# Kernel tuning notes

Measured on AMD Instinct MI355X. Metric: run time of the kernel, lower is better.

Reference implementation:

```python
import jax, jax.numpy as jnp
import numpy as np

N_CB = 10          # n_codebooks
K = 2048           # codebook_size
D = 256            # codebook_dim
SEM = 256          # semantic_proj_dim
W2V = 1024         # w2v_bert_dim
COMMIT = 0.25      # commitment_cost


def setup_inputs() -> dict:
    key = jax.random.key(0)
    ks = jax.random.split(key, 7)
    B, T = 16, 1024
    z = jax.random.normal(ks[0], (B, T, D), jnp.float32)
    w2v_targets = jax.random.normal(ks[1], (B, T, W2V), jnp.float32)
    # codebooks: uniform(-1/K, 1/K) as in nn.init.uniform_
    E = jax.random.uniform(ks[2], (N_CB, K, D), jnp.float32, -1.0 / K, 1.0 / K)
    # semantic head: Linear(D, SEM) -> GELU -> Linear(SEM, W2V)
    W1 = jax.random.normal(ks[3], (D, SEM), jnp.float32) * (1.0 / np.sqrt(D))
    b1 = jnp.zeros((SEM,), jnp.float32)
    W2 = jax.random.normal(ks[4], (SEM, W2V), jnp.float32) * (1.0 / np.sqrt(SEM))
    b2 = jnp.zeros((W2V,), jnp.float32)
    return {"z": z, "w2v_targets": w2v_targets, "E": E,
            "W1": W1, "b1": b1, "W2": W2, "b2": b2}


def _vq_step(residual, Ei):
    """Single-codebook VQ with straight-through estimator.
    residual: (B,T,D); Ei: (K,D). Returns (z_q, indices, loss)."""
    sg = jax.lax.stop_gradient
    B, T, d = residual.shape
    flat = residual.reshape(-1, d)                      # (N, D)
    dist = (jnp.sum(flat * flat, axis=1, keepdims=True)
            - 2.0 * flat @ Ei.T
            + jnp.sum(Ei * Ei, axis=1))
    idx = jnp.argmin(dist, axis=1).reshape(B, T)        # (B, T)
    q = Ei[idx]                                         # (B, T, D) gather
    commitment_loss = jnp.mean((sg(q) - residual) ** 2)
    embedding_loss = jnp.mean((q - sg(residual)) ** 2)
    loss = embedding_loss + COMMIT * commitment_loss
    z_q = residual + sg(q - residual)                   # straight-through
    return z_q, idx, loss


def reference(z, w2v_targets, E, W1, b1, W2, b2):
    residual = z
    z_q_total = jnp.zeros_like(z)
    codes = []
    vq_loss = jnp.float32(0.0)
    semantic_loss = jnp.float32(0.0)
    for i in range(N_CB):
        z_q_i, idx_i, loss_i = _vq_step(residual, E[i])
        if i == 0:
            # semantic head on CB1 output (torch GELU default = exact erf)
            h = jax.nn.gelu(z_q_i @ W1 + b1, approximate=False)
            predicted = h @ W2 + b2                     # (B, T, W2V)
            semantic_loss = jnp.mean((predicted - w2v_targets) ** 2)
        z_q_total = z_q_total + z_q_i
        residual = residual - jax.lax.stop_gradient(z_q_i)
        vq_loss = vq_loss + loss_i
        codes.append(idx_i)
    all_codes = jnp.stack(codes, axis=-1)               # (B, T, N_CB)
    return z_q_total, all_codes, vq_loss, semantic_loss
```

## Files before the change

### kernel.cpp

```cpp
#include <hip/hip_runtime.h>
#include <float.h>
#include <math.h>

#define NTOK 16384
#define KCB  2048
#define DDIM 256
#define NCB  10
#define MARGIN 5.0e-4f

typedef __attribute__((ext_vector_type(8))) short  short8;
typedef __attribute__((ext_vector_type(4))) float  f32x4;

static __device__ __forceinline__ unsigned short f2bf(float f) {
    unsigned int b = __float_as_uint(f);
    unsigned int r = b + 0x7FFFu + ((b >> 16) & 1u);
    return (unsigned short)(r >> 16);
}

__global__ __launch_bounds__(256) void prep_all(const float* __restrict__ E,
                                                const float* __restrict__ z,
                                                const float* __restrict__ W1,
                                                const float* __restrict__ W2,
                                                float* __restrict__ sseE,
                                                float* __restrict__ normA,
                                                unsigned short* __restrict__ Eh,
                                                unsigned short* __restrict__ resH,
                                                unsigned short* __restrict__ w1t,
                                                unsigned short* __restrict__ w2t) {
    const int b = blockIdx.x;
    if (b < 9216) {
        const float* src; unsigned short* dst; int i;
        if (b < 5120) { src = E; dst = Eh;   i = b * 256 + threadIdx.x; }
        else          { src = z; dst = resH; i = (b - 5120) * 256 + threadIdx.x; }
        float4 f = *(const float4*)(src + (size_t)i * 4);
        unsigned short h[4] = { f2bf(f.x), f2bf(f.y), f2bf(f.z), f2bf(f.w) };
        *(ushort4*)(dst + (size_t)i * 4) = *(ushort4*)h;
    } else if (b < 9472) {
        int j = (b - 9216) * 256 + threadIdx.x;
        int n = j >> 8, k = j & 255;
        w1t[j] = f2bf(W1[k * 256 + n]);
    } else if (b < 10496) {
        int j = (b - 9472) * 256 + threadIdx.x;
        int n = j >> 8, k = j & 255;
        w2t[j] = f2bf(W2[k * 1024 + n]);
    } else {
        const int gw   = ((b - 10496) * 256 + threadIdx.x) >> 6;
        const int lane = threadIdx.x & 63;
        const int row  = gw * 4 + (lane >> 4);
        const int l    = lane & 15;
        const float* src = nullptr; float* dst = nullptr;
        if (row < NCB * KCB)             { src = E + (size_t)row * DDIM;               dst = sseE + row; }
        else if (row < NCB * KCB + NTOK) { src = z + (size_t)(row - NCB * KCB) * DDIM; dst = normA + (row - NCB * KCB); }
        float r = 0.f;
        if (src) {
            const float* a = src + ((l >> 3) << 7) + (l & 7);
            float v = a[0];
            r = __fmul_rn(v, v);
            #pragma unroll
            for (int k = 1; k < 16; ++k) { v = a[k * 8]; r = __fadd_rn(r, __fmul_rn(v, v)); }
        }
        r = __fadd_rn(r, __shfl_xor(r, 1, 64));
        r = __fadd_rn(r, __shfl_xor(r, 2, 64));
        r = __fadd_rn(r, __shfl_xor(r, 4, 64));
        r = __fadd_rn(r, __shfl_xor(r, 8, 64));
        if (src && l == 0) *dst = r;
    }
}

__global__ __launch_bounds__(256) void vq_screen(const unsigned short* __restrict__ resH,
                                                 const unsigned short* __restrict__ Ehi,
                                                 const float* __restrict__ sseEi,
                                                 int2* __restrict__ gSlots,
                                                 int* __restrict__ gCnt,
                                                 float* __restrict__ gMin) {
    __shared__ unsigned short sBh[2][128 * 40];
    __shared__ float sC[128];
    __shared__ int   lCnt[128];
    __shared__ int2  lSlot[128][4];
    const int tid = threadIdx.x;
    const int wv = tid >> 6, lane = tid & 63;
    const int l15 = lane & 15, qd = lane >> 4;
    const int tile = blockIdx.x >> 4, slice = blockIdx.x & 15;
    const int t0 = tile * 128, c0 = slice * 128;

    if (tid < 128) { lCnt[tid] = 0; sC[tid] = sseEi[c0 + tid]; }
    {
        int2 inf; inf.x = 0x7F800000; inf.y = 0;
        ((int2*)lSlot)[tid] = inf; ((int2*)lSlot)[tid + 256] = inf;
    }

    f32x4 acc[2][8];
    #pragma unroll
    for (int m = 0; m < 2; ++m)
        #pragma unroll
        for (int n = 0; n < 8; ++n) acc[m][n] = (f32x4){0.f, 0.f, 0.f, 0.f};

    const size_t rowA0 = (size_t)(t0 + wv * 32 + l15) * 256 + qd * 8;
    short8 ah0 = *(const short8*)(resH + rowA0);
    short8 ah1 = *(const short8*)(resH + rowA0 + 16 * 256);
    #pragma unroll
    for (int jj = 0; jj < 2; ++jj) {
        int f = jj * 256 + tid;
        int r = f >> 2, cc = (f & 3) * 8;
        *(uint4*)(sBh[0] + r * 40 + cc) = *(const uint4*)(Ehi + (size_t)(c0 + r) * 256 + cc);
    }
    __syncthreads();

    for (int kc = 0; kc < 8; ++kc) {
        const int cur = kc & 1;
        short8 an0, an1;
        if (kc < 7) {
            const int dbn = (kc + 1) * 32;
            an0 = *(const short8*)(resH + rowA0 + dbn);
            an1 = *(const short8*)(resH + rowA0 + 16 * 256 + dbn);
            #pragma unroll
            for (int jj = 0; jj < 2; ++jj) {
                int f = jj * 256 + tid;
                int r = f >> 2, cc = (f & 3) * 8;
                *(uint4*)(sBh[cur ^ 1] + r * 40 + cc) =
                    *(const uint4*)(Ehi + (size_t)(c0 + r) * 256 + dbn + cc);
            }
        }
        #pragma unroll
        for (int n = 0; n < 8; ++n) {
            short8 bh = *(const short8*)(sBh[cur] + (n * 16 + l15) * 40 + qd * 8);
            acc[0][n] = __builtin_amdgcn_mfma_f32_16x16x32_bf16(ah0, bh, acc[0][n], 0, 0, 0);
            acc[1][n] = __builtin_amdgcn_mfma_f32_16x16x32_bf16(ah1, bh, acc[1][n], 0, 0, 0);
        }
        __syncthreads();
        if (kc < 7) { ah0 = an0; ah1 = an1; }
    }

    #pragma unroll
    for (int m = 0; m < 2; ++m)
        #pragma unroll
        for (int n = 0; n < 8; ++n) {
            float Cv = sC[n * 16 + l15];
            #pragma unroll
            for (int r = 0; r < 4; ++r) acc[m][n][r] = fmaf(-2.f, acc[m][n][r], Cv);
        }
    #pragma unroll
    for (int m = 0; m < 2; ++m)
        #pragma unroll
        for (int r = 0; r < 4; ++r) {
            float v = acc[m][0][r];
            #pragma unroll
            for (int n = 1; n < 8; ++n) v = fminf(v, acc[m][n][r]);
            v = fminf(v, __shfl_xor(v, 1, 64));
            v = fminf(v, __shfl_xor(v, 2, 64));
            v = fminf(v, __shfl_xor(v, 4, 64));
            v = fminf(v, __shfl_xor(v, 8, 64));
            int tloc = wv * 32 + m * 16 + qd * 4 + r;
            if (l15 == 0) gMin[(t0 + tloc) * 16 + slice] = v;
            float thr = v + MARGIN;
            #pragma unroll
            for (int n = 0; n < 8; ++n) {
                float sv = acc[m][n][r];
                if (sv <= thr) {
                    int pos = atomicAdd(&lCnt[tloc], 1);
                    if (pos < 4) {
                        int2 e; e.x = __float_as_int(sv); e.y = c0 + n * 16 + l15;
                        lSlot[tloc][pos] = e;
                    }
                }
            }
        }
    __syncthreads();
    {
        int tloc = tid >> 1, half = tid & 1;
        size_t base = (size_t)(t0 + tloc) * 64 + slice * 4 + half * 2;
        gSlots[base]     = lSlot[tloc][half * 2];
        gSlots[base + 1] = lSlot[tloc][half * 2 + 1];
        if (!half) gCnt[(t0 + tloc) * 16 + slice] = lCnt[tloc];
    }
}

static __device__ __forceinline__ float np_chain(const float* __restrict__ sRow,
                                                 const float* __restrict__ Ei,
                                                 int cc, float A, float C) {
    const float4* e = (const float4*)(Ei + (size_t)cc * DDIM);
    float a = 0.f;
    #pragma unroll 8
    for (int k = 0; k < 64; ++k) {
        float4 ev = e[k];
        const float4 rv = *(const float4*)(sRow + k * 4);
        a = fmaf(rv.x, ev.x, a); a = fmaf(rv.y, ev.y, a);
        a = fmaf(rv.z, ev.z, a); a = fmaf(rv.w, ev.w, a);
    }
    return __fadd_rn(fmaf(-2.f, a, A), C);
}

__global__ __launch_bounds__(256) void vq_post(const float* __restrict__ resSrc,
                                               const float* __restrict__ Ei,
                                               const float* __restrict__ sseEi,
                                               float* __restrict__ res,
                                               float* __restrict__ zq,
                                               float* __restrict__ codes,
                                               float* __restrict__ lossPart,
                                               float* __restrict__ normA,
                                               unsigned short* __restrict__ resHp,
                                               unsigned short* __restrict__ zqb,
                                               const int2* __restrict__ gSlots,
                                               const int* __restrict__ gCnt,
                                               const float* __restrict__ gMin,
                                               int iter) {
    __shared__ float sScr[4][4][256];
    const int tid = threadIdx.x;
    const int wv = tid >> 6, lane = tid & 63;
    const int g = lane >> 4, l15 = lane & 15;
    const int tb = blockIdx.x * 16 + wv * 4;
    float lsum = 0.f;

    int2 sl[4]; float4 r4[4]; int cnt4[4]; float smin4[4]; float4 zq4[4]; float A4[4];
    #pragma unroll
    for (int j = 0; j < 4; ++j) sl[j] = gSlots[(size_t)(tb + j) * 64 + lane];
    #pragma unroll
    for (int j = 0; j < 4; ++j)
        r4[j] = *(const float4*)(resSrc + (size_t)(tb + j) * DDIM + lane * 4);
    #pragma unroll
    for (int j = 0; j < 4; ++j) cnt4[j]  = (lane < 16) ? gCnt[(tb + j) * 16 + lane] : 0;
    #pragma unroll
    for (int j = 0; j < 4; ++j) smin4[j] = (lane < 16) ? gMin[(tb + j) * 16 + lane] : FLT_MAX;
    #pragma unroll
    for (int j = 0; j < 4; ++j) A4[j] = normA[tb + j];
    if (iter > 0) {
        #pragma unroll
        for (int j = 0; j < 4; ++j)
            zq4[j] = *(const float4*)(zq + (size_t)(tb + j) * DDIM + lane * 4);
    }

    int winner[4];
    #pragma unroll
    for (int j = 0; j < 4; ++j) {
        float gm = smin4[j];
        #pragma unroll
        for (int o = 32; o >= 1; o >>= 1) gm = fminf(gm, __shfl_xor(gm, o, 64));
        const float thr = gm + MARGIN;
        float sv = __int_as_float(sl[j].x);
        unsigned long long bal = __ballot((sv <= thr) ? 1 : 0);
        bool ovfRel = __any((lane < 16 && cnt4[j] > 4 && smin4[j] <= thr) ? 1 : 0);
        if (!ovfRel && __popcll(bal) == 1) {
            winner[j] = __shfl(sl[j].y, __ffsll(bal) - 1, 64);
        } else if (!ovfRel) {
            *(float4*)(&sScr[wv][j][lane * 4]) = r4[j];
            const bool qal = (sv <= thr);
            const int cc = qal ? sl[j].y : 0;
            float s = np_chain(sScr[wv][j], Ei, cc, A4[j], sseEi[cc]);
            unsigned long long best = qal
                ? (((unsigned long long)__float_as_uint(s) << 32) | (unsigned)cc)
                : ~0ULL;
            #pragma unroll
            for (int o = 32; o >= 1; o >>= 1) {
                unsigned long long ot = __shfl_xor(best, o, 64);
                if (ot < best) best = ot;
            }
            winner[j] = (int)(unsigned)(best & 0xFFFFFFFFu);
        } else {
            *(float4*)(&sScr[wv][j][lane * 4]) = r4[j];
            unsigned long long best = ~0ULL;
            for (int cc = lane; cc < KCB; cc += 64) {
                float s = np_chain(sScr[wv][j], Ei, cc, A4[j], sseEi[cc]);
                unsigned long long key =
                    ((unsigned long long)__float_as_uint(s) << 32) | (unsigned)cc;
                if (key < best) best = key;
            }
            #pragma unroll
            for (int o = 32; o >= 1; o >>= 1) {
                unsigned long long ot = __shfl_xor(best, o, 64);
                if (ot < best) best = ot;
            }
            winner[j] = (int)(unsigned)(best & 0xFFFFFFFFu);
        }
    }
    #pragma unroll
    for (int j = 0; j < 4; ++j)
        if (lane == j) codes[(size_t)(tb + j) * NCB + iter] = (float)winner[j];

    float4 q4[4];
    #pragma unroll
    for (int j = 0; j < 4; ++j)
        q4[j] = *(const float4*)(Ei + (size_t)winner[j] * DDIM + lane * 4);

    #pragma unroll
    for (int j = 0; j < 4; ++j) {
        const size_t go = (size_t)(tb + j) * DDIM + lane * 4;
        float4 rn4, zqi4;
        float tqx = q4[j].x - r4[j].x; zqi4.x = r4[j].x + tqx; rn4.x = r4[j].x - zqi4.x;
        float tqy = q4[j].y - r4[j].y; zqi4.y = r4[j].y + tqy; rn4.y = r4[j].y - zqi4.y;
        float tqz = q4[j].z - r4[j].z; zqi4.z = r4[j].z + tqz; rn4.z = r4[j].z - zqi4.z;
        float tqw = q4[j].w - r4[j].w; zqi4.w = r4[j].w + tqw; rn4.w = r4[j].w - zqi4.w;
        lsum = fmaf(tqx, tqx, lsum); lsum = fmaf(tqy, tqy, lsum);
        lsum = fmaf(tqz, tqz, lsum); lsum = fmaf(tqw, tqw, lsum);
        *(float4*)(res + go) = rn4;
        {
            unsigned short h[4] = { f2bf(rn4.x), f2bf(rn4.y), f2bf(rn4.z), f2bf(rn4.w) };
            *(ushort4*)(resHp + go) = *(ushort4*)h;
        }
        if (iter == 0) {
            *(float4*)(zq + go) = zqi4;
            unsigned short u[4] = { f2bf(zqi4.x), f2bf(zqi4.y), f2bf(zqi4.z), f2bf(zqi4.w) };
            *(ushort4*)(zqb + go) = *(ushort4*)u;
        } else {
            zq4[j].x += zqi4.x; zq4[j].y += zqi4.y;
            zq4[j].z += zqi4.z; zq4[j].w += zqi4.w;
            *(float4*)(zq + go) = zq4[j];
        }
        *(float4*)(&sScr[wv][j][lane * 4]) = rn4;
    }
    {
        const float* a = &sScr[wv][g][((l15 >> 3) << 7) + (l15 & 7)];
        float v = a[0];
        float r = __fmul_rn(v, v);
        #pragma unroll
        for (int k = 1; k < 16; ++k) { v = a[k * 8]; r = __fadd_rn(r, __fmul_rn(v, v)); }
        r = __fadd_rn(r, __shfl_xor(r, 1, 64));
        r = __fadd_rn(r, __shfl_xor(r, 2, 64));
        r = __fadd_rn(r, __shfl_xor(r, 4, 64));
        r = __fadd_rn(r, __shfl_xor(r, 8, 64));
        if (l15 == 0) normA[tb + g] = r;
    }
    #pragma unroll
    for (int o = 32; o >= 1; o >>= 1) lsum += __shfl_xor(lsum, o, 64);
    if (lane == 0) lossPart[iter * 4096 + blockIdx.x * 4 + wv] = lsum;
}

__global__ __launch_bounds__(256) void sem_mfma(const unsigned short* __restrict__ zqb,
                                                const float* __restrict__ tgt,
                                                const unsigned short* __restrict__ w1t,
                                                const float* __restrict__ b1,
                                                const unsigned short* __restrict__ w2t,
                                                const float* __restrict__ b2,
                                                float* __restrict__ semPart) {
    __shared__ uint4 sBq[2048];
    __shared__ uint4 sHq[2048];
    char* sBb = (char*)sBq;
    char* sHb = (char*)sHq;
    const int tid = threadIdx.x;
    const int wv = tid >> 6, lane = tid & 63;
    const int l15 = lane & 15, qd = lane >> 4;
    const int tb = (blockIdx.x >> 1) * 64;
    const int oh = blockIdx.x & 1;
    const int rs = tid >> 5, cs = tid & 31;
    const int swzs = (cs * 16) ^ ((rs & 7) << 4);

    #pragma unroll
    for (int j = 0; j < 8; ++j) {
        int r = j * 8 + rs;
        *(uint4*)(sHb + r * 512 + swzs) = *(const uint4*)(zqb + (size_t)(tb + r) * 256 + cs * 8);
    }
    __syncthreads();
    short8 az[8];
    {
        const int R = wv * 16 + l15;
        #pragma unroll
        for (int kc = 0; kc < 8; ++kc)
            az[kc] = *(const short8*)(sHb + R * 512 + ((kc * 64 + qd * 16) ^ ((R & 7) << 4)));
    }
    __syncthreads();

    #pragma unroll 1
    for (int s1 = 0; s1 < 4; ++s1) {
        #pragma unroll
        for (int j = 0; j < 8; ++j) {
            int r = j * 8 + rs;
            *(uint4*)(sBb + r * 512 + swzs) = *(const uint4*)(w1t + (size_t)(s1 * 64 + r) * 256 + cs * 8);
        }
        __syncthreads();
        f32x4 acc[4];
        #pragma unroll
        for (int n = 0; n < 4; ++n) acc[n] = (f32x4){0.f, 0.f, 0.f, 0.f};
        for (int kc = 0; kc < 8; ++kc) {
            #pragma unroll
            for (int n = 0; n < 4; ++n) {
                const int R = n * 16 + l15;
                short8 b = *(const short8*)(sBb + R * 512 + ((kc * 64 + qd * 16) ^ ((R & 7) << 4)));
                acc[n] = __builtin_amdgcn_mfma_f32_16x16x32_bf16(az[kc], b, acc[n], 0, 0, 0);
            }
        }
        #pragma unroll
        for (int n = 0; n < 4; ++n) {
            const int o = s1 * 64 + n * 16 + l15;
            const float b1v = b1[o];
            #pragma unroll
            for (int r = 0; r < 4; ++r) {
                float x = acc[n][r] + b1v;
                const int tr = wv * 16 + qd * 4 + r;
                *(unsigned short*)(sHb + tr * 512 + ((o * 2) ^ ((tr & 7) << 4))) =
                    f2bf(0.5f * x * (1.f + erff(x * 0.70710678f)));
            }
        }
        __syncthreads();
    }

    short8 ah[8];
    {
        const int R = wv * 16 + l15;
        #pragma unroll
        for (int kc = 0; kc < 8; ++kc)
            ah[kc] = *(const short8*)(sHb + R * 512 + ((kc * 64 + qd * 16) ^ ((R & 7) << 4)));
    }
    #pragma unroll
    for (int j = 0; j < 8; ++j) {
        int r = j * 8 + rs;
        *(uint4*)(sBb + r * 512 + swzs) = *(const uint4*)(w2t + (size_t)(oh * 512 + r) * 256 + cs * 8);
    }
    __syncthreads();

    float lsum = 0.f;
    #pragma unroll 1
    for (int s2 = 0; s2 < 8; ++s2) {
        const int gs = oh * 8 + s2;
        char* cb = (s2 & 1) ? sHb : sBb;
        char* nb = (s2 & 1) ? sBb : sHb;
        if (s2 < 7) {
            #pragma unroll
            for (int j = 0; j < 8; ++j) {
                int r = j * 8 + rs;
                *(uint4*)(nb + r * 512 + swzs) =
                    *(const uint4*)(w2t + (size_t)((gs + 1) * 64 + r) * 256 + cs * 8);
            }
        }
        float tg[4][4], b2v[4];
        #pragma unroll
        for (int n = 0; n < 4; ++n) {
            const int o = gs * 64 + n * 16 + l15;
            b2v[n] = b2[o];
            #pragma unroll
            for (int r = 0; r < 4; ++r)
                tg[n][r] = tgt[(size_t)(tb + wv * 16 + qd * 4 + r) * 1024 + o];
        }
        f32x4 acc[4];
        #pragma unroll
        for (int n = 0; n < 4; ++n) acc[n] = (f32x4){0.f, 0.f, 0.f, 0.f};
        for (int kc = 0; kc < 8; ++kc) {
            #pragma unroll
            for (int n = 0; n < 4; ++n) {
                const int R = n * 16 + l15;
                short8 b = *(const short8*)(cb + R * 512 + ((kc * 64 + qd * 16) ^ ((R & 7) << 4)));
                acc[n] = __builtin_amdgcn_mfma_f32_16x16x32_bf16(ah[kc], b, acc[n], 0, 0, 0);
            }
        }
        #pragma unroll
        for (int n = 0; n < 4; ++n)
            #pragma unroll
            for (int r = 0; r < 4; ++r) {
                float dv = (acc[n][r] + b2v[n]) - tg[n][r];
                lsum = fmaf(dv, dv, lsum);
            }
        __syncthreads();
    }
    #pragma unroll
    for (int o = 32; o >= 1; o >>= 1) lsum += __shfl_xor(lsum, o, 64);
    if (lane == 0) semPart[blockIdx.x * 4 + wv] = lsum;
}

__global__ __launch_bounds__(256) void loss_final(const float* __restrict__ lossPart,
                                                  const float* __restrict__ semPart,
                                                  float* __restrict__ vql) {
    __shared__ float sRed[4], sRed2[4];
    float s = 0.f, q = 0.f;
    for (int i = threadIdx.x; i < 40960; i += 256) s += lossPart[i];
    for (int i = threadIdx.x; i < 2048; i += 256) q += semPart[i];
    #pragma unroll
    for (int o = 32; o >= 1; o >>= 1) { s += __shfl_xor(s, o, 64); q += __shfl_xor(q, o, 64); }
    if ((threadIdx.x & 63) == 0) { sRed[threadIdx.x >> 6] = s; sRed2[threadIdx.x >> 6] = q; }
    __syncthreads();
    if (threadIdx.x == 0) {
        vql[0] = (sRed[0] + sRed[1] + sRed[2] + sRed[3]) * (1.25f / 4194304.f);
        vql[1] = (sRed2[0] + sRed2[1] + sRed2[2] + sRed2[3]) * (1.0f / 16777216.f);
    }
}

extern "C" void kernel_launch(void* const* d_in, const int* in_sizes, int n_in,
                              void* d_out, int out_size, void* d_ws, size_t ws_size,
                              hipStream_t stream) {
    const float* z   = (const float*)d_in[0];
    const float* tgt = (const float*)d_in[1];
    const float* E   = (const float*)d_in[2];
    const float* W1  = (const float*)d_in[3];
    const float* b1  = (const float*)d_in[4];
    const float* W2  = (const float*)d_in[5];
    const float* b2  = (const float*)d_in[6];

    float* out   = (float*)d_out;
    float* zq    = out;
    float* codes = out + (size_t)NTOK * DDIM;
    float* vql   = codes + (size_t)NTOK * NCB;

    char* w = (char*)d_ws;
    float*          res   = (float*)(w);
    unsigned short* resH  = (unsigned short*)(w + 16777216);
    float*          semPart=(float*)(w + 25165824);
    unsigned short* Eh    = (unsigned short*)(w + 33554432);
    unsigned short* zqb   = (unsigned short*)(w + 54525952);
    int2*           gSlots= (int2*)(w + 62914560);
    int*            gCnt  = (int*)(w + 71303168);
    float*          gMin  = (float*)(w + 72351744);
    float*          sseE  = (float*)(w + 73400320);
    float*          normA = (float*)(w + 73531392);
    float*          lossPart=(float*)(w + 73662464);
    unsigned short* w1t   = (unsigned short*)(w + 73924608);
    unsigned short* w2t   = (unsigned short*)(w + 74055680);

    prep_all<<<12800, 256, 0, stream>>>(E, z, W1, W2, sseE, normA, Eh, resH, w1t, w2t);
    for (int it = 0; it < NCB; ++it) {
        const float*          Ei    = E  + (size_t)it * KCB * DDIM;
        const unsigned short* Ehi   = Eh + (size_t)it * KCB * DDIM;
        const float*          sseEi = sseE + (size_t)it * KCB;
        const float* resSrc = (it == 0) ? z : res;
        vq_screen<<<2048, 256, 0, stream>>>(resH, Ehi, sseEi, gSlots, gCnt, gMin);
        vq_post<<<1024, 256, 0, stream>>>(resSrc, Ei, sseEi, res, zq, codes, lossPart,
                                          normA, resH, zqb, gSlots, gCnt, gMin, it);
        if (it == 0)
            sem_mfma<<<512, 256, 0, stream>>>(zqb, tgt, w1t, b1, w2t, b2, semPart);
    }
    loss_final<<<1, 256, 0, stream>>>(lossPart, semPart, vql);
}
```

Baseline: 976.9 us.

## Fuse norm computation into bf16 prep and drop gMin/gCnt buffers

The prep kernel now computes the squared norms of codebook rows and tokens from the tile it already loads, staged through shared memory, instead of a second pass that re-reads E and z. The screening kernel no longer writes per-slice minima and counts. The post kernel instead takes the global minimum from the slot values and reads an overflow flag packed into the high bit of a slot index. The screen kernel's block order is also remapped, interleaving by eight, which may improve cache locality. Together these cut global memory traffic and launch work, but the overflow check is now coarser: any slice overflow forces the full fallback, even one that is not near the minimum.

New measurement: 2.916 ms. +198.5%, slower.

```diff
diff --git a/kernel.cpp b/kernel.cpp
--- a/kernel.cpp
+++ b/kernel.cpp
@@ -7,6 +7,7 @@
 #define DDIM 256
 #define NCB  10
 #define MARGIN 5.0e-4f
+#define OVF_FLAG (1 << 30)
 
 typedef __attribute__((ext_vector_type(8))) short  short8;
 typedef __attribute__((ext_vector_type(4))) float  f32x4;
@@ -29,50 +30,46 @@
                                                 unsigned short* __restrict__ w2t) {
     const int b = blockIdx.x;
     if (b < 9216) {
-        const float* src; unsigned short* dst; int i;
-        if (b < 5120) { src = E; dst = Eh;   i = b * 256 + threadIdx.x; }
-        else          { src = z; dst = resH; i = (b - 5120) * 256 + threadIdx.x; }
+        __shared__ float sRow[4][260];
+        const float* src; unsigned short* dst; float* ndst; int i, row0;
+        if (b < 5120) { src = E; dst = Eh;   ndst = sseE;  i = b * 256 + threadIdx.x;          row0 = b * 4; }
+        else          { src = z; dst = resH; ndst = normA; i = (b - 5120) * 256 + threadIdx.x; row0 = (b - 5120) * 4; }
         float4 f = *(const float4*)(src + (size_t)i * 4);
         unsigned short h[4] = { f2bf(f.x), f2bf(f.y), f2bf(f.z), f2bf(f.w) };
         *(ushort4*)(dst + (size_t)i * 4) = *(ushort4*)h;
+        {
+            int r = threadIdx.x >> 6, c = (threadIdx.x & 63) * 4;
+            *(float4*)&sRow[r][c] = f;
+        }
+        __syncthreads();
+        if (threadIdx.x < 64) {
+            const int l15 = threadIdx.x & 15, g = threadIdx.x >> 4;
+            const float* a = &sRow[g][((l15 >> 3) << 7) + (l15 & 7)];
+            float v = a[0];
+            float r = __fmul_rn(v, v);
+            #pragma unroll
+            for (int k = 1; k < 16; ++k) { v = a[k * 8]; r = __fadd_rn(r, __fmul_rn(v, v)); }
+            r = __fadd_rn(r, __shfl_xor(r, 1, 64));
+            r = __fadd_rn(r, __shfl_xor(r, 2, 64));
+            r = __fadd_rn(r, __shfl_xor(r, 4, 64));
+            r = __fadd_rn(r, __shfl_xor(r, 8, 64));
+            if (l15 == 0) ndst[row0 + g] = r;
+        }
     } else if (b < 9472) {
         int j = (b - 9216) * 256 + threadIdx.x;
         int n = j >> 8, k = j & 255;
         w1t[j] = f2bf(W1[k * 256 + n]);
-    } else if (b < 10496) {
+    } else {
         int j = (b - 9472) * 256 + threadIdx.x;
         int n = j >> 8, k = j & 255;
         w2t[j] = f2bf(W2[k * 1024 + n]);
-    } else {
-        const int gw   = ((b - 10496) * 256 + threadIdx.x) >> 6;
-        const int lane = threadIdx.x & 63;
-        const int row  = gw * 4 + (lane >> 4);
-        const int l    = lane & 15;
-        const float* src = nullptr; float* dst = nullptr;
-        if (row < NCB * KCB)             { src = E + (size_t)row * DDIM;               dst = sseE + row; }
-        else if (row < NCB * KCB + NTOK) { src = z + (size_t)(row - NCB * KCB) * DDIM; dst = normA + (row - NCB * KCB); }
-        float r = 0.f;
-        if (src) {
-            const float* a = src + ((l >> 3) << 7) + (l & 7);
-            float v = a[0];
-            r = __fmul_rn(v, v);
-            #pragma unroll
-            for (int k = 1; k < 16; ++k) { v = a[k * 8]; r = __fadd_rn(r, __fmul_rn(v, v)); }
-        }
-        r = __fadd_rn(r, __shfl_xor(r, 1, 64));
-        r = __fadd_rn(r, __shfl_xor(r, 2, 64));
-        r = __fadd_rn(r, __shfl_xor(r, 4, 64));
-        r = __fadd_rn(r, __shfl_xor(r, 8, 64));
-        if (src && l == 0) *dst = r;
     }
 }
 
 __global__ __launch_bounds__(256) void vq_screen(const unsigned short* __restrict__ resH,
                                                  const unsigned short* __restrict__ Ehi,
                                                  const float* __restrict__ sseEi,
-                                                 int2* __restrict__ gSlots,
-                                                 int* __restrict__ gCnt,
-                                                 float* __restrict__ gMin) {
+                                                 int2* __restrict__ gSlots) {
     __shared__ unsigned short sBh[2][128 * 40];
     __shared__ float sC[128];
     __shared__ int   lCnt[128];
@@ -80,7 +77,8 @@
     const int tid = threadIdx.x;
     const int wv = tid >> 6, lane = tid & 63;
     const int l15 = lane & 15, qd = lane >> 4;
-    const int tile = blockIdx.x >> 4, slice = blockIdx.x & 15;
+    const int wid = (blockIdx.x & 7) * 256 + (blockIdx.x >> 3);
+    const int tile = wid >> 4, slice = wid & 15;
     const int t0 = tile * 128, c0 = slice * 128;
 
     if (tid < 128) { lCnt[tid] = 0; sC[tid] = sseEi[c0 + tid]; }
@@ -151,7 +149,6 @@
             v = fminf(v, __shfl_xor(v, 4, 64));
             v = fminf(v, __shfl_xor(v, 8, 64));
             int tloc = wv * 32 + m * 16 + qd * 4 + r;
-            if (l15 == 0) gMin[(t0 + tloc) * 16 + slice] = v;
             float thr = v + MARGIN;
             #pragma unroll
             for (int n = 0; n < 8; ++n) {
@@ -169,9 +166,11 @@
     {
         int tloc = tid >> 1, half = tid & 1;
         size_t base = (size_t)(t0 + tloc) * 64 + slice * 4 + half * 2;
-        gSlots[base]     = lSlot[tloc][half * 2];
-        gSlots[base + 1] = lSlot[tloc][half * 2 + 1];
-        if (!half) gCnt[(t0 + tloc) * 16 + slice] = lCnt[tloc];
+        int2 s0 = lSlot[tloc][half * 2];
+        int2 s1 = lSlot[tloc][half * 2 + 1];
+        if (half && lCnt[tloc] > 4) s1.y |= OVF_FLAG;
+        gSlots[base]     = s0;
+        gSlots[base + 1] = s1;
     }
 }
 
@@ -201,8 +200,6 @@
                                                unsigned short* __restrict__ resHp,
                                                unsigned short* __restrict__ zqb,
                                                const int2* __restrict__ gSlots,
-                                               const int* __restrict__ gCnt,
-                                               const float* __restrict__ gMin,
                                                int iter) {
     __shared__ float sScr[4][4][256];
     const int tid = threadIdx.x;
@@ -211,17 +208,13 @@
     const int tb = blockIdx.x * 16 + wv * 4;
     float lsum = 0.f;
 
-    int2 sl[4]; float4 r4[4]; int cnt4[4]; float smin4[4]; float4 zq4[4]; float A4[4];
+    int2 sl[4]; float4 r4[4]; float4 zq4[4]; float A4[4];
     #pragma unroll
     for (int j = 0; j < 4; ++j) sl[j] = gSlots[(size_t)(tb + j) * 64 + lane];
     #pragma unroll
     for (int j = 0; j < 4; ++j)
         r4[j] = *(const float4*)(resSrc + (size_t)(tb + j) * DDIM + lane * 4);
     #pragma unroll
-    for (int j = 0; j < 4; ++j) cnt4[j]  = (lane < 16) ? gCnt[(tb + j) * 16 + lane] : 0;
-    #pragma unroll
-    for (int j = 0; j < 4; ++j) smin4[j] = (lane < 16) ? gMin[(tb + j) * 16 + lane] : FLT_MAX;
-    #pragma unroll
     for (int j = 0; j < 4; ++j) A4[j] = normA[tb + j];
     if (iter > 0) {
         #pragma unroll
@@ -232,16 +225,16 @@
     int winner[4];
     #pragma unroll
     for (int j = 0; j < 4; ++j) {
-        float gm = smin4[j];
+        const float sv = __int_as_float(sl[j].x);
+        float gm = sv;
         #pragma unroll
         for (int o = 32; o >= 1; o >>= 1) gm = fminf(gm, __shfl_xor(gm, o, 64));
         const float thr = gm + MARGIN;
-        float sv = __int_as_float(sl[j].x);
+        const bool ovf = __any(((lane & 3) == 3 && (sl[j].y & OVF_FLAG)) ? 1 : 0);
         unsigned long long bal = __ballot((sv <= thr) ? 1 : 0);
-        bool ovfRel = __any((lane < 16 && cnt4[j] > 4 && smin4[j] <= thr) ? 1 : 0);
-        if (!ovfRel && __popcll(bal) == 1) {
+        if (!ovf && __popcll(bal) == 1) {
             winner[j] = __shfl(sl[j].y, __ffsll(bal) - 1, 64);
-        } else if (!ovfRel) {
+        } else if (!ovf) {
             *(float4*)(&sScr[wv][j][lane * 4]) = r4[j];
             const bool qal = (sv <= thr);
             const int cc = qal ? sl[j].y : 0;
@@ -494,23 +487,21 @@
     unsigned short* Eh    = (unsigned short*)(w + 33554432);
     unsigned short* zqb   = (unsigned short*)(w + 54525952);
     int2*           gSlots= (int2*)(w + 62914560);
-    int*            gCnt  = (int*)(w + 71303168);
-    float*          gMin  = (float*)(w + 72351744);
     float*          sseE  = (float*)(w + 73400320);
     float*          normA = (float*)(w + 73531392);
     float*          lossPart=(float*)(w + 73662464);
     unsigned short* w1t   = (unsigned short*)(w + 73924608);
     unsigned short* w2t   = (unsigned short*)(w + 74055680);
 
-    prep_all<<<12800, 256, 0, stream>>>(E, z, W1, W2, sseE, normA, Eh, resH, w1t, w2t);
+    prep_all<<<10496, 256, 0, stream>>>(E, z, W1, W2, sseE, normA, Eh, resH, w1t, w2t);
     for (int it = 0; it < NCB; ++it) {
         const float*          Ei    = E  + (size_t)it * KCB * DDIM;
         const unsigned short* Ehi   = Eh + (size_t)it * KCB * DDIM;
         const float*          sseEi = sseE + (size_t)it * KCB;
         const float* resSrc = (it == 0) ? z : res;
-        vq_screen<<<2048, 256, 0, stream>>>(resH, Ehi, sseEi, gSlots, gCnt, gMin);
+        vq_screen<<<2048, 256, 0, stream>>>(resH, Ehi, sseEi, gSlots);
         vq_post<<<1024, 256, 0, stream>>>(resSrc, Ei, sseEi, res, zq, codes, lossPart,
-                                          normA, resH, zqb, gSlots, gCnt, gMin, it);
+                                          normA, resH, zqb, gSlots, it);
         if (it == 0)
             sem_mfma<<<512, 256, 0, stream>>>(zqb, tgt, w1t, b1, w2t, b2, semPart);
     }
```
